# Kernel optimization log

Hardware: AMD Instinct MI355X
Metric: run time of the kernel (lower is better)

The kernel has to match this reference:

```python
import jax, jax.numpy as jnp
import numpy as np

N_NODES = 50000
N_EDGES = 800000
DIM = 128
N_HEADS = 8
HEAD_DIM = DIM // N_HEADS
LN_EPS = 1e-5
NEG_SLOPE = 0.2


def setup_inputs() -> dict:
    key = jax.random.key(0)
    ks = jax.random.split(key, 10)
    inp = {
        "x": jax.random.normal(ks[0], (N_NODES, DIM), dtype=jnp.float32),
        "src": jax.random.randint(ks[1], (N_EDGES,), 0, N_NODES, dtype=jnp.int32),
        "dst": jax.random.randint(ks[2], (N_EDGES,), 0, N_NODES, dtype=jnp.int32),
        "ln_gamma": jnp.ones((DIM,), dtype=jnp.float32),
        "ln_beta": jnp.zeros((DIM,), dtype=jnp.float32),
        "W_in": jax.random.normal(ks[3], (DIM, DIM), dtype=jnp.float32) * (DIM ** -0.5),
        "b_in": jax.random.normal(ks[4], (DIM,), dtype=jnp.float32) * 0.02,
        "W_u": jax.random.normal(ks[5], (DIM, N_HEADS), dtype=jnp.float32) * (DIM ** -0.5),
        "b_u": jax.random.normal(ks[6], (N_HEADS,), dtype=jnp.float32) * 0.02,
        "W_v": jax.random.normal(ks[7], (DIM, N_HEADS), dtype=jnp.float32) * (DIM ** -0.5),
        "W_ff": jax.random.normal(ks[8], (DIM, DIM), dtype=jnp.float32) * (DIM ** -0.5),
        "b_ff": jax.random.normal(ks[9], (DIM,), dtype=jnp.float32) * 0.02,
    }
    return inp


def _gat_forward(x, src, dst, ln_gamma, ln_beta, W_in, b_in, W_u, b_u, W_v, W_ff, b_ff):
    # LayerNorm over feature dim
    mu = jnp.mean(x, axis=-1, keepdims=True)
    var = jnp.mean(jnp.square(x - mu), axis=-1, keepdims=True)
    x = (x - mu) * jax.lax.rsqrt(var + LN_EPS) * ln_gamma + ln_beta

    # input linear
    x = x @ W_in + b_in                      # [N, D]

    # per-node attention score pieces
    scores_u = x @ W_u + b_u                 # [N, H]
    scores_v = x @ W_v                       # [N, H]

    # u_add_v: gather to edges (u = src, v = dst)
    e = scores_u[src] + scores_v[dst]        # [E, H]
    e = jnp.where(e >= 0, e, NEG_SLOPE * e)  # LeakyReLU(0.2)

    # edge_softmax: softmax over incoming edges of each destination node
    m = jax.ops.segment_max(e, dst, num_segments=N_NODES)   # [N, H]
    ex = jnp.exp(e - m[dst])                                 # [E, H]
    s = jax.ops.segment_sum(ex, dst, num_segments=N_NODES)   # [N, H]
    probs = ex / s[dst]                                      # [E, H]

    # u_mul_e_sum: weighted neighbor aggregation
    xh = x.reshape(N_NODES, HEAD_DIM, N_HEADS)                # [N, hd, H]
    msg = xh[src] * probs[:, None, :]                         # [E, hd, H]
    agg = jax.ops.segment_sum(msg, dst, num_segments=N_NODES) # [N, hd, H]
    out = agg.reshape(N_NODES, DIM)

    # feed-forward (dropout p=0 -> identity)
    return out @ W_ff + b_ff


def reference(x, src, dst, ln_gamma, ln_beta, W_in, b_in, W_u, b_u, W_v, W_ff, b_ff):
    return _gat_forward(x, src, dst, ln_gamma, ln_beta, W_in, b_in, W_u, b_u, W_v, W_ff, b_ff)
```

## Files before the change

kernel.cpp:

```cpp
#include <hip/hip_runtime.h>

#define N_NODES 50000
#define N_EDGES 800000
#define DIM 128
#define H 8
#define PAD 64

typedef unsigned short ushort_t;
typedef unsigned int uint_t;
typedef __attribute__((ext_vector_type(8))) short bf16x8;
typedef __attribute__((ext_vector_type(4))) float f32x4;

__device__ __forceinline__ float bf2f(ushort_t u) {
    return __uint_as_float(((uint_t)u) << 16);
}
__device__ __forceinline__ ushort_t f2bf(float f) {
    uint_t x = __float_as_uint(f);
    uint_t r = (x + 0x7FFFu + ((x >> 16) & 1u)) >> 16;
    return (ushort_t)r;
}

template<bool DO_LN, bool BF16_OUT, bool DO_SCORES>
__global__ __launch_bounds__(256) void k_gemm_mfma(
    const float* __restrict__ X, const ushort_t* __restrict__ Ab,
    const float* __restrict__ W, const float* __restrict__ bias,
    const float* __restrict__ gamma, const float* __restrict__ beta,
    const float* __restrict__ W_u, const float* __restrict__ b_u,
    const float* __restrict__ W_v,
    float* __restrict__ Yf, ushort_t* __restrict__ Yb,
    float* __restrict__ su, float* __restrict__ sv)
{
    __shared__ ushort_t wt[128 * 128];
    __shared__ float    wuvT[2][8 * 128];

    const int t  = threadIdx.x;
    const int n0 = blockIdx.x * 64;
    const int l  = t & 63, w = t >> 6;
    const int m  = l & 15, q = l >> 4;

    #pragma unroll 4
    for (int rep = 0; rep < 16; ++rep) {
        int id = rep * 256 + t;
        int k  = id >> 5;
        int n4 = (id & 31) << 2;
        float4 wv = *(const float4*)(W + (size_t)k * DIM + n4);
        int kb = k >> 3, kj = k & 7;
        wt[(n4+0)*128 + ((kb ^ ((n4+0) & 15)) << 3) + kj] = f2bf(wv.x);
        wt[(n4+1)*128 + ((kb ^ ((n4+1) & 15)) << 3) + kj] = f2bf(wv.y);
        wt[(n4+2)*128 + ((kb ^ ((n4+2) & 15)) << 3) + kj] = f2bf(wv.z);
        wt[(n4+3)*128 + ((kb ^ ((n4+3) & 15)) << 3) + kj] = f2bf(wv.w);
    }
    if (DO_SCORES) {
        #pragma unroll
        for (int i = 0; i < 8; ++i) {
            int g = i * 256 + t;
            int sel = g >> 10;
            int rem = g & 1023;
            int col = rem >> 3, h = rem & 7;
            float v = sel ? W_v[rem] : W_u[rem];
            wuvT[sel][h * 128 + col] = v;
        }
    }

    const int node = n0 + w * 16 + m;
    const int nc   = (node < N_NODES) ? node : (N_NODES - 1);
    bf16x8 afrag[4];

    if (DO_LN) {
        const float* xrow = X + (size_t)nc * DIM;
        float xv[4][8];
        float s = 0.f, ss = 0.f;
        #pragma unroll
        for (int ks = 0; ks < 4; ++ks) {
            int base = 32 * ks + 8 * q;
            float4 a0 = *(const float4*)(xrow + base);
            float4 a1 = *(const float4*)(xrow + base + 4);
            xv[ks][0]=a0.x; xv[ks][1]=a0.y; xv[ks][2]=a0.z; xv[ks][3]=a0.w;
            xv[ks][4]=a1.x; xv[ks][5]=a1.y; xv[ks][6]=a1.z; xv[ks][7]=a1.w;
            #pragma unroll
            for (int j = 0; j < 8; ++j) { s += xv[ks][j]; ss += xv[ks][j]*xv[ks][j]; }
        }
        s  += __shfl_xor(s, 16);  s  += __shfl_xor(s, 32);
        ss += __shfl_xor(ss, 16); ss += __shfl_xor(ss, 32);
        float mu   = s * (1.f / DIM);
        float var  = ss * (1.f / DIM) - mu * mu;
        float rstd = rsqrtf(var + 1e-5f);
        #pragma unroll
        for (int ks = 0; ks < 4; ++ks) {
            int base = 32 * ks + 8 * q;
            float4 g0 = *(const float4*)(gamma + base);
            float4 g1 = *(const float4*)(gamma + base + 4);
            float4 b0 = *(const float4*)(beta + base);
            float4 b1 = *(const float4*)(beta + base + 4);
            float gg[8] = {g0.x,g0.y,g0.z,g0.w,g1.x,g1.y,g1.z,g1.w};
            float bb[8] = {b0.x,b0.y,b0.z,b0.w,b1.x,b1.y,b1.z,b1.w};
            #pragma unroll
            for (int j = 0; j < 8; ++j) {
                float xn = (xv[ks][j] - mu) * rstd * gg[j] + bb[j];
                afrag[ks][j] = (short)f2bf(xn);
            }
        }
    } else {
        const ushort_t* arow = Ab + (size_t)nc * DIM;
        #pragma unroll
        for (int ks = 0; ks < 4; ++ks)
            afrag[ks] = *(const bf16x8*)(arow + 32 * ks + 8 * q);
    }

    __syncthreads();

    f32x4 acc[8];
    #pragma unroll
    for (int c = 0; c < 8; ++c) acc[c] = (f32x4){0.f, 0.f, 0.f, 0.f};

    #pragma unroll
    for (int ks = 0; ks < 4; ++ks) {
        int k8 = ks * 4 + q;
        #pragma unroll
        for (int c = 0; c < 8; ++c) {
            int n = c * 16 + m;
            bf16x8 bfrag = *(const bf16x8*)(wt + n * 128 + ((k8 ^ m) << 3));
            acc[c] = __builtin_amdgcn_mfma_f32_16x16x32_bf16(afrag[ks], bfrag, acc[c], 0, 0, 0);
        }
    }

    float bcol[8];
    #pragma unroll
    for (int c = 0; c < 8; ++c) bcol[c] = bias[c * 16 + m];

    #pragma unroll
    for (int r = 0; r < 4; ++r) {
        int nn = n0 + w * 16 + q * 4 + r;
        bool ok = (nn < N_NODES);
        float v[8];
        #pragma unroll
        for (int c = 0; c < 8; ++c) v[c] = acc[c][r] + bcol[c];

        if (ok) {
            #pragma unroll
            for (int c = 0; c < 8; ++c) {
                int col = c * 16 + m;
                if (BF16_OUT) Yb[(size_t)nn * DIM + col] = f2bf(v[c]);
                else          Yf[(size_t)nn * DIM + col] = v[c];
            }
        }

        if (DO_SCORES) {
            float ps[16];
            #pragma unroll
            for (int h = 0; h < 8; ++h) {
                float a = 0.f, b = 0.f;
                #pragma unroll
                for (int c = 0; c < 8; ++c) {
                    int col = c * 16 + m;
                    a += v[c] * wuvT[0][h * 128 + col];
                    b += v[c] * wuvT[1][h * 128 + col];
                }
                ps[h] = a; ps[8 + h] = b;
            }
            #pragma unroll
            for (int o = 1; o < 16; o <<= 1) {
                #pragma unroll
                for (int j = 0; j < 16; ++j) ps[j] += __shfl_xor(ps[j], o);
            }
            if (ok) {
                if (m < 8) su[nn * H + m] = ps[m] + b_u[m];
                else       sv[nn * H + (m - 8)] = ps[m];
            }
        }
    }
}

__global__ __launch_bounds__(256) void k_zero(int* __restrict__ deg)
{
    int i = blockIdx.x * 256 + threadIdx.x;
    if (i < N_NODES) deg[i] = 0;
}

__global__ __launch_bounds__(256) void k_build(
    const int* __restrict__ src, const int* __restrict__ dst,
    int* __restrict__ deg, ushort_t* __restrict__ esrc_p)
{
    int e = blockIdx.x * 256 + threadIdx.x;
    if (e < N_EDGES) {
        int d = dst[e];
        int pos = atomicAdd(&deg[d], 1);
        if (pos < PAD) esrc_p[(size_t)d * PAD + pos] = (ushort_t)src[e];
    }
}

__global__ __launch_bounds__(128) void k_node_agg(
    const ushort_t* __restrict__ esrc_p, const int* __restrict__ deg,
    const float* __restrict__ su, const float* __restrict__ sv,
    const ushort_t* __restrict__ yb, ushort_t* __restrict__ aggb)
{
    const int w = threadIdx.x >> 6, l = threadIdx.x & 63;
    const int n = blockIdx.x * 2 + w;
    const int d = min(deg[n], PAD);
    const int hp = 2 * (l & 3);
    const float2 svp = *(const float2*)(sv + n * H + hp);
    const int sl = (l < d) ? (int)esrc_p[(size_t)n * PAD + l] : 0;

    float ssum0 = 0.f, ssum1 = 0.f, acc0 = 0.f, acc1 = 0.f;
    int i = 0;
    for (; i + 4 <= d; i += 4) {
        int s0 = __shfl(sl, i);
        int s1 = __shfl(sl, i + 1);
        int s2 = __shfl(sl, i + 2);
        int s3 = __shfl(sl, i + 3);
        float2 u0 = *(const float2*)(su + s0 * H + hp);
        float2 u1 = *(const float2*)(su + s1 * H + hp);
        float2 u2 = *(const float2*)(su + s2 * H + hp);
        float2 u3 = *(const float2*)(su + s3 * H + hp);
        uint_t y0 = *(const uint_t*)(yb + (size_t)s0 * DIM + 2 * l);
        uint_t y1 = *(const uint_t*)(yb + (size_t)s1 * DIM + 2 * l);
        uint_t y2 = *(const uint_t*)(yb + (size_t)s2 * DIM + 2 * l);
        uint_t y3 = *(const uint_t*)(yb + (size_t)s3 * DIM + 2 * l);

        float e0x = u0.x + svp.x; e0x = (e0x >= 0.f) ? e0x : 0.2f * e0x;
        float e0y = u0.y + svp.y; e0y = (e0y >= 0.f) ? e0y : 0.2f * e0y;
        float e1x = u1.x + svp.x; e1x = (e1x >= 0.f) ? e1x : 0.2f * e1x;
        float e1y = u1.y + svp.y; e1y = (e1y >= 0.f) ? e1y : 0.2f * e1y;
        float e2x = u2.x + svp.x; e2x = (e2x >= 0.f) ? e2x : 0.2f * e2x;
        float e2y = u2.y + svp.y; e2y = (e2y >= 0.f) ? e2y : 0.2f * e2y;
        float e3x = u3.x + svp.x; e3x = (e3x >= 0.f) ? e3x : 0.2f * e3x;
        float e3y = u3.y + svp.y; e3y = (e3y >= 0.f) ? e3y : 0.2f * e3y;

        float w0x = __expf(e0x), w0y = __expf(e0y);
        float w1x = __expf(e1x), w1y = __expf(e1y);
        float w2x = __expf(e2x), w2y = __expf(e2y);
        float w3x = __expf(e3x), w3y = __expf(e3y);

        ssum0 += (w0x + w1x) + (w2x + w3x);
        ssum1 += (w0y + w1y) + (w2y + w3y);
        acc0 += w0x * bf2f((ushort_t)(y0 & 0xFFFF)) + w1x * bf2f((ushort_t)(y1 & 0xFFFF))
              + w2x * bf2f((ushort_t)(y2 & 0xFFFF)) + w3x * bf2f((ushort_t)(y3 & 0xFFFF));
        acc1 += w0y * bf2f((ushort_t)(y0 >> 16)) + w1y * bf2f((ushort_t)(y1 >> 16))
              + w2y * bf2f((ushort_t)(y2 >> 16)) + w3y * bf2f((ushort_t)(y3 >> 16));
    }
    for (; i < d; ++i) {
        int s0 = __shfl(sl, i);
        float2 u0 = *(const float2*)(su + s0 * H + hp);
        uint_t y0 = *(const uint_t*)(yb + (size_t)s0 * DIM + 2 * l);
        float e0x = u0.x + svp.x; e0x = (e0x >= 0.f) ? e0x : 0.2f * e0x;
        float e0y = u0.y + svp.y; e0y = (e0y >= 0.f) ? e0y : 0.2f * e0y;
        float w0x = __expf(e0x), w0y = __expf(e0y);
        ssum0 += w0x; ssum1 += w0y;
        acc0 += w0x * bf2f((ushort_t)(y0 & 0xFFFF));
        acc1 += w0y * bf2f((ushort_t)(y0 >> 16));
    }
    float r0 = (ssum0 > 0.f) ? (1.0f / ssum0) : 0.f;
    float r1 = (ssum1 > 0.f) ? (1.0f / ssum1) : 0.f;
    uint_t o = (uint_t)f2bf(acc0 * r0) | ((uint_t)f2bf(acc1 * r1) << 16);
    *(uint_t*)(aggb + (size_t)n * DIM + 2 * l) = o;
}

extern "C" void kernel_launch(void* const* d_in, const int* in_sizes, int n_in,
                              void* d_out, int out_size, void* d_ws, size_t ws_size,
                              hipStream_t stream)
{
    const float* x     = (const float*)d_in[0];
    const int*   src   = (const int*)  d_in[1];
    const int*   dst   = (const int*)  d_in[2];
    const float* gamma = (const float*)d_in[3];
    const float* beta  = (const float*)d_in[4];
    const float* W_in  = (const float*)d_in[5];
    const float* b_in  = (const float*)d_in[6];
    const float* W_u   = (const float*)d_in[7];
    const float* b_u   = (const float*)d_in[8];
    const float* W_v   = (const float*)d_in[9];
    const float* W_ff  = (const float*)d_in[10];
    const float* b_ff  = (const float*)d_in[11];
    float* out = (float*)d_out;

    char* ws = (char*)d_ws;
    ushort_t* yb     = (ushort_t*)ws; ws += (size_t)N_NODES * DIM * 2;
    ushort_t* aggb   = (ushort_t*)ws; ws += (size_t)N_NODES * DIM * 2;
    float* su        = (float*)ws; ws += (size_t)N_NODES * H * 4;
    float* sv        = (float*)ws; ws += (size_t)N_NODES * H * 4;
    int*   deg       = (int*)  ws; ws += (size_t)N_NODES * 4;
    ushort_t* esrc_p = (ushort_t*)ws; ws += (size_t)N_NODES * PAD * 2;

    const int NB_NODE = (N_NODES + 255) / 256;
    const int NB_EDGE = (N_EDGES + 255) / 256;
    const int NB_GEMM = (N_NODES + 63) / 64;

    hipLaunchKernelGGL(k_zero, dim3(NB_NODE), dim3(256), 0, stream, deg);
    hipLaunchKernelGGL((k_gemm_mfma<true, true, true>), dim3(NB_GEMM), dim3(256), 0, stream,
                       x, (const ushort_t*)nullptr, W_in, b_in, gamma, beta,
                       W_u, b_u, W_v,
                       (float*)nullptr, yb, su, sv);
    hipLaunchKernelGGL(k_build, dim3(NB_EDGE), dim3(256), 0, stream,
                       src, dst, deg, esrc_p);
    hipLaunchKernelGGL(k_node_agg, dim3(N_NODES / 2), dim3(128), 0, stream,
                       esrc_p, deg, su, sv, yb, aggb);
    hipLaunchKernelGGL((k_gemm_mfma<false, false, false>), dim3(NB_GEMM), dim3(256), 0, stream,
                       (const float*)nullptr, aggb, W_ff, b_ff,
                       (const float*)nullptr, (const float*)nullptr,
                       (const float*)nullptr, (const float*)nullptr, (const float*)nullptr,
                       out, (ushort_t*)nullptr, (float*)nullptr, (float*)nullptr);
}
```

Measured before the change: 238.2 us.

## Replace global atomic CSR build with two-pass partitioned bucketing in LDS

The per-edge global atomicAdd into deg and the scattered 2-byte writes into esrc_p are replaced by a two-stage partition sort. The first kernel bins edges by destination partition using shared-memory histograms and one global atomic per partition per block. The second kernel builds each partition's padded neighbor lists in LDS and writes them out coalesced, along with degrees. This is meant to cut global atomic contention and uncoalesced scatter, at the cost of an extra pass over an intermediate buffer and a fixed partition capacity that silently drops edges if a partition holds more than 4096.

```diff
diff --git a/kernel.cpp b/kernel.cpp
--- a/kernel.cpp
+++ b/kernel.cpp
@@ -5,6 +5,10 @@
 #define DIM 128
 #define H 8
 #define PAD 64
+#define NPART 256
+#define PART_NODES 196
+#define PART_CAP 4096
+#define EPB 2048
 
 typedef unsigned short ushort_t;
 typedef unsigned int uint_t;
@@ -171,21 +175,84 @@
     }
 }
 
-__global__ __launch_bounds__(256) void k_zero(int* __restrict__ deg)
-{
-    int i = blockIdx.x * 256 + threadIdx.x;
-    if (i < N_NODES) deg[i] = 0;
-}
-
-__global__ __launch_bounds__(256) void k_build(
+__global__ __launch_bounds__(256) void k_zero(int* __restrict__ pcount)
+{
+    pcount[threadIdx.x] = 0;
+}
+
+__global__ __launch_bounds__(256) void k_part(
     const int* __restrict__ src, const int* __restrict__ dst,
-    int* __restrict__ deg, ushort_t* __restrict__ esrc_p)
-{
-    int e = blockIdx.x * 256 + threadIdx.x;
-    if (e < N_EDGES) {
-        int d = dst[e];
-        int pos = atomicAdd(&deg[d], 1);
-        if (pos < PAD) esrc_p[(size_t)d * PAD + pos] = (ushort_t)src[e];
+    int* __restrict__ pcount, uint_t* __restrict__ pbuf)
+{
+    __shared__ int hist[NPART];
+    __shared__ int base[NPART];
+    __shared__ uint_t rec[EPB];
+    __shared__ ushort_t rnk[EPB];
+    __shared__ unsigned char prt[EPB];
+
+    const int t = threadIdx.x;
+    const int e0 = blockIdx.x * EPB;
+    hist[t] = 0;
+    __syncthreads();
+
+    #pragma unroll
+    for (int i = 0; i < EPB / 256; ++i) {
+        int idx = i * 256 + t;
+        int e = e0 + idx;
+        if (e < N_EDGES) {
+            int s = src[e], d = dst[e];
+            int p = d / PART_NODES;
+            int dl = d - p * PART_NODES;
+            int r = atomicAdd(&hist[p], 1);
+            rec[idx] = ((uint_t)dl << 16) | (uint_t)s;
+            rnk[idx] = (ushort_t)r;
+            prt[idx] = (unsigned char)p;
+        }
+    }
+    __syncthreads();
+    base[t] = atomicAdd(&pcount[t], hist[t]);
+    __syncthreads();
+
+    #pragma unroll
+    for (int i = 0; i < EPB / 256; ++i) {
+        int idx = i * 256 + t;
+        int e = e0 + idx;
+        if (e < N_EDGES) {
+            int p = prt[idx];
+            int slot = base[p] + (int)rnk[idx];
+            if (slot < PART_CAP)
+                pbuf[(size_t)p * PART_CAP + slot] = rec[idx];
+        }
+    }
+}
+
+__global__ __launch_bounds__(256) void k_bucket(
+    const uint_t* __restrict__ pbuf, const int* __restrict__ pcount,
+    ushort_t* __restrict__ esrc_p, int* __restrict__ deg)
+{
+    __shared__ ushort_t buck[PART_NODES * PAD];
+    __shared__ int cnt[PART_NODES];
+
+    const int p = blockIdx.x, t = threadIdx.x;
+    for (int i = t; i < PART_NODES; i += 256) cnt[i] = 0;
+    __syncthreads();
+
+    const int m = min(pcount[p], PART_CAP);
+    for (int i = t; i < m; i += 256) {
+        uint_t v = pbuf[(size_t)p * PART_CAP + i];
+        int dl = (int)(v >> 16);
+        int pos = atomicAdd(&cnt[dl], 1);
+        if (pos < PAD) buck[dl * PAD + pos] = (ushort_t)(v & 0xFFFF);
+    }
+    __syncthreads();
+
+    const int n0 = p * PART_NODES;
+    const uint_t* b32 = (const uint_t*)buck;
+    uint_t* g32 = (uint_t*)(esrc_p + (size_t)n0 * PAD);
+    for (int i = t; i < PART_NODES * PAD / 2; i += 256) g32[i] = b32[i];
+    for (int i = t; i < PART_NODES; i += 256) {
+        int n = n0 + i;
+        if (n < N_NODES) deg[n] = cnt[i];
     }
 }
 
@@ -279,19 +346,22 @@
     float* su        = (float*)ws; ws += (size_t)N_NODES * H * 4;
     float* sv        = (float*)ws; ws += (size_t)N_NODES * H * 4;
     int*   deg       = (int*)  ws; ws += (size_t)N_NODES * 4;
-    ushort_t* esrc_p = (ushort_t*)ws; ws += (size_t)N_NODES * PAD * 2;
-
-    const int NB_NODE = (N_NODES + 255) / 256;
-    const int NB_EDGE = (N_EDGES + 255) / 256;
+    int*   pcount    = (int*)  ws; ws += (size_t)NPART * 4;
+    uint_t* pbuf     = (uint_t*)ws; ws += (size_t)NPART * PART_CAP * 4;
+    ushort_t* esrc_p = (ushort_t*)ws; ws += (size_t)NPART * PART_NODES * PAD * 2;
+
+    const int NB_PART = (N_EDGES + EPB - 1) / EPB;
     const int NB_GEMM = (N_NODES + 63) / 64;
 
-    hipLaunchKernelGGL(k_zero, dim3(NB_NODE), dim3(256), 0, stream, deg);
+    hipLaunchKernelGGL(k_zero, dim3(1), dim3(256), 0, stream, pcount);
     hipLaunchKernelGGL((k_gemm_mfma<true, true, true>), dim3(NB_GEMM), dim3(256), 0, stream,
                        x, (const ushort_t*)nullptr, W_in, b_in, gamma, beta,
                        W_u, b_u, W_v,
                        (float*)nullptr, yb, su, sv);
-    hipLaunchKernelGGL(k_build, dim3(NB_EDGE), dim3(256), 0, stream,
-                       src, dst, deg, esrc_p);
+    hipLaunchKernelGGL(k_part, dim3(NB_PART), dim3(256), 0, stream,
+                       src, dst, pcount, pbuf);
+    hipLaunchKernelGGL(k_bucket, dim3(NPART), dim3(256), 0, stream,
+                       pbuf, pcount, esrc_p, deg);
     hipLaunchKernelGGL(k_node_agg, dim3(N_NODES / 2), dim3(128), 0, stream,
                        esrc_p, deg, su, sv, yb, aggb);
     hipLaunchKernelGGL((k_gemm_mfma<false, false, false>), dim3(NB_GEMM), dim3(256), 0, stream,
```

Result: faster. 215.8 us (-9.4%).
